# Kernel optimization log

Hardware: AMD Instinct MI355X
Metric: run time of the kernel (lower is better)

Reference implementation:

```python
import jax, jax.numpy as jnp
import numpy as np

B, T, H = 64, 1024, 1024


def setup_inputs() -> dict:
    key = jax.random.key(0)
    ks = jax.random.split(key, 8)
    s = 1.0 / np.sqrt(H)
    return {
        "spatial_feats": jax.random.normal(ks[0], (B, T, H), dtype=jnp.float32),
        "hidden_state": jax.random.normal(ks[1], (B, H), dtype=jnp.float32),
        "W_enc": jax.random.uniform(ks[2], (H, H), jnp.float32, -s, s),
        "b_enc": jax.random.uniform(ks[3], (H,), jnp.float32, -s, s),
        "W_dec": jax.random.uniform(ks[4], (H, H), jnp.float32, -s, s),
        "b_dec": jax.random.uniform(ks[5], (H,), jnp.float32, -s, s),
        "w_score": jax.random.uniform(ks[6], (H,), jnp.float32, -s, s),
        "b_score": jax.random.uniform(ks[7], (), jnp.float32, -s, s),
    }


def reference(spatial_feats, hidden_state, W_enc, b_enc, W_dec, b_dec, w_score, b_score):
    # decoder_proj(hidden_state): [B, H] -> [B, 1, H]
    dec = (jnp.einsum("bh,oh->bo", hidden_state, W_dec) + b_dec)[:, None, :]
    # encoder_proj(spatial_feats): [B, T, H]
    enc = jnp.einsum("bth,oh->bto", spatial_feats, W_enc) + b_enc
    energy = jnp.tanh(enc + dec)                      # [B, T, H]
    scores = jnp.einsum("bth,h->bt", energy, w_score) + b_score  # [B, T]
    weights = jax.nn.softmax(scores, axis=1)          # [B, T]
    context = jnp.einsum("bth,bt->bh", spatial_feats, weights)   # [B, H]
    return (context, weights)
```

## Files before the change

### kernel.cpp

```cpp
#include <hip/hip_runtime.h>
#include <hip/hip_bf16.h>
#include <math.h>


typedef __attribute__((ext_vector_type(8))) short bf16x8;
typedef __attribute__((ext_vector_type(8))) unsigned short ushort8;
typedef __attribute__((ext_vector_type(4))) float f32x4;

__device__ __forceinline__ unsigned short f2bf(float f) {
  union { float f; unsigned int u; } v; v.f = f;
  unsigned int r = v.u + 0x7FFFu + ((v.u >> 16) & 1u);
  return (unsigned short)(r >> 16);
}

__device__ __forceinline__ float bf2f(unsigned short b) {
  union { unsigned int u; float f; } v; v.u = ((unsigned int)b) << 16;
  return v.f;
}

__device__ __forceinline__ float fast_tanh(float x) {
  float e = __expf(2.0f * x);
  return 1.0f - 2.0f / (e + 1.0f);
}

__device__ __forceinline__ void gld16(const void* g, void* l) {
  __builtin_amdgcn_global_load_lds(
      (const __attribute__((address_space(1))) void*)g,
      (__attribute__((address_space(3))) void*)l, 16, 0, 0);
}

__global__ __launch_bounds__(256) void prep_kernel(
    const float* __restrict__ spatial, const float* __restrict__ hidden,
    const float* __restrict__ W_enc, const float* __restrict__ b_enc,
    const float* __restrict__ W_dec, const float* __restrict__ b_dec,
    unsigned short* __restrict__ Wbf, unsigned short* __restrict__ Abf,
    float* __restrict__ dec, int nCvt) {
  __shared__ float hs[1024];
  const int bid = blockIdx.x, tid = threadIdx.x;
  if (bid < nCvt) {
    const bool isW = bid < 32;
    const float* src = isW ? W_enc : spatial;
    unsigned short* dst = isW ? Wbf : Abf;
    const size_t base = (size_t)(isW ? bid : bid - 32) * 8192 + tid;
    #pragma unroll 4
    for (int i = 0; i < 32; i++) {
      size_t g4 = base + (size_t)i * 256;
      float4 v = ((const float4*)src)[g4];
      ushort4 o;
      o.x = f2bf(v.x); o.y = f2bf(v.y); o.z = f2bf(v.z); o.w = f2bf(v.w);
      *(ushort4*)(dst + g4 * 4) = o;
    }
    return;
  }
  const int dbid = bid - nCvt;
  const int b = dbid >> 3, o0 = (dbid & 7) * 128;
  const int wave = tid >> 6, lane = tid & 63;
  ((float4*)hs)[tid] = ((const float4*)(hidden + (size_t)b * 1024))[tid];
  __syncthreads();
  for (int it = 0; it < 32; it++) {
    int o = o0 + it * 4 + wave;
    const float4* w4 = (const float4*)(W_dec + (size_t)o * 1024);
    float4 acc; acc.x = acc.y = acc.z = acc.w = 0.f;
    #pragma unroll
    for (int j = 0; j < 4; j++) {
      int i = j * 64 + lane;
      float4 x = ((const float4*)hs)[i], y = w4[i];
      acc.x = fmaf(x.x, y.x, acc.x);
      acc.y = fmaf(x.y, y.y, acc.y);
      acc.z = fmaf(x.z, y.z, acc.z);
      acc.w = fmaf(x.w, y.w, acc.w);
    }
    float v = (acc.x + acc.y) + (acc.z + acc.w);
    #pragma unroll
    for (int off = 1; off < 64; off <<= 1) v += __shfl_xor(v, off);
    if (lane == 0) dec[b * 1024 + o] = v + b_dec[o] + b_enc[o];
  }
}

__global__ __launch_bounds__(256) void enc_score_bf16_kernel(
    const unsigned short* __restrict__ A,
    const unsigned short* __restrict__ W,
    const float* __restrict__ dec,
    const float* __restrict__ w_score,
    float* __restrict__ scores_p)
{
  __shared__ unsigned short As[3][128][32];
  __shared__ unsigned short Bs[3][128][32];

  const int bid = blockIdx.x;
  const int swz = (bid & 7) * 512 + (bid >> 3);
  const int n0 = (swz & 7) * 128;
  const int m0 = (swz >> 3) * 128;
  const int tid = threadIdx.x;
  const int lane = tid & 63, wave = tid >> 6;
  const int wm = (wave >> 1) * 64, wn = (wave & 1) * 64;
  const int quad = lane >> 4, colL = lane & 15;

  const int srow = wave * 32 + (lane >> 2);
  const int scol = (lane & 3) * 8;
  const unsigned short* ga = A + (size_t)(m0 + srow) * 1024 + scol;
  const unsigned short* gb = W + (size_t)(n0 + srow) * 1024 + scol;
  unsigned short* la = &As[0][0][0] + wave * 1024;
  unsigned short* lb = &Bs[0][0][0] + wave * 1024;

  f32x4 acc[4][4];
  #pragma unroll
  for (int mi = 0; mi < 4; mi++)
    #pragma unroll
    for (int ni = 0; ni < 4; ni++)
      acc[mi][ni] = (f32x4){0.f, 0.f, 0.f, 0.f};

  auto stage_tile = [&](int t, int b) {
    const unsigned short* ga_ = ga + t * 32;
    const unsigned short* gb_ = gb + t * 32;
    unsigned short* la_ = la + b * 4096;
    unsigned short* lb_ = lb + b * 4096;
    gld16(ga_,             la_);
    gld16(ga_ + 16 * 1024, la_ + 512);
    gld16(gb_,             lb_);
    gld16(gb_ + 16 * 1024, lb_ + 512);
  };

  auto compute_tile = [&](int b) {
    bf16x8 af[4], bfr[4];
    #pragma unroll
    for (int i = 0; i < 4; i++) {
      af[i]  = *(const bf16x8*)(&As[b][wm + i * 16 + colL][quad * 8]);
      bfr[i] = *(const bf16x8*)(&Bs[b][wn + i * 16 + colL][quad * 8]);
    }
    __builtin_amdgcn_s_setprio(1);
    #pragma unroll
    for (int mi = 0; mi < 4; mi++)
      #pragma unroll
      for (int ni = 0; ni < 4; ni++)
        acc[mi][ni] = __builtin_amdgcn_mfma_f32_16x16x32_bf16(
            af[mi], bfr[ni], acc[mi][ni], 0, 0, 0);
    __builtin_amdgcn_s_setprio(0);
  };

  stage_tile(0, 0);
  stage_tile(1, 1);

  int buf = 0;
  for (int t = 0; t < 31; t++) {
    asm volatile("s_waitcnt vmcnt(4)" ::: "memory");
    __builtin_amdgcn_s_barrier();
    if (t < 30) {
      int b2 = buf + 2; if (b2 >= 3) b2 -= 3;
      stage_tile(t + 2, b2);
    }
    compute_tile(buf);
    buf = (buf == 2) ? 0 : buf + 1;
  }
  asm volatile("s_waitcnt vmcnt(0)" ::: "memory");
  __builtin_amdgcn_s_barrier();
  compute_tile(buf);

  const int b = m0 >> 10;
  float decv[4], wsv[4];
  #pragma unroll
  for (int ni = 0; ni < 4; ni++) {
    int n = n0 + wn + ni * 16 + colL;
    decv[ni] = dec[b * 1024 + n];
    wsv[ni] = w_score[n];
  }
  const int slot = (swz & 7) * 2 + (wave & 1);
  #pragma unroll
  for (int mi = 0; mi < 4; mi++) {
    float rs[4] = {0.f, 0.f, 0.f, 0.f};
    #pragma unroll
    for (int ni = 0; ni < 4; ni++)
      #pragma unroll
      for (int r = 0; r < 4; r++)
        rs[r] += fast_tanh(acc[mi][ni][r] + decv[ni]) * wsv[ni];
    #pragma unroll
    for (int r = 0; r < 4; r++) {
      float v = rs[r];
      v += __shfl_xor(v, 1);
      v += __shfl_xor(v, 2);
      v += __shfl_xor(v, 4);
      v += __shfl_xor(v, 8);
      if (colL == 0)
        scores_p[slot * 65536 + m0 + wm + mi * 16 + quad * 4 + r] = v;
    }
  }
}

__global__ __launch_bounds__(256) void enc_score_f32_kernel(
    const float* __restrict__ A, const float* __restrict__ W,
    const float* __restrict__ dec, const float* __restrict__ w_score,
    float* __restrict__ scores_p) {
  __shared__ unsigned short As[128][32];
  __shared__ unsigned short Bs[128][32];
  const int bid = blockIdx.x;
  const int n0 = (bid & 7) * 128;
  const int m0 = (bid >> 3) * 128;
  const int tid = threadIdx.x;
  const int lane = tid & 63, wave = tid >> 6;
  const int wm = (wave >> 1) * 64, wn = (wave & 1) * 64;
  const int quad = lane >> 4, colL = lane & 15;
  const int srow = tid >> 3;
  const int scol = (tid & 7) * 4;
  f32x4 acc[4][4];
  #pragma unroll
  for (int mi = 0; mi < 4; mi++)
    #pragma unroll
    for (int ni = 0; ni < 4; ni++)
      acc[mi][ni] = (f32x4){0.f, 0.f, 0.f, 0.f};
  for (int k0 = 0; k0 < 1024; k0 += 32) {
    #pragma unroll
    for (int p = 0; p < 4; p++) {
      int r = p * 32 + srow;
      float4 va = *(const float4*)(A + (size_t)(m0 + r) * 1024 + (k0 + scol));
      float4 vb = *(const float4*)(W + (size_t)(n0 + r) * 1024 + (k0 + scol));
      ushort4 pa, pb;
      pa.x = f2bf(va.x); pa.y = f2bf(va.y); pa.z = f2bf(va.z); pa.w = f2bf(va.w);
      pb.x = f2bf(vb.x); pb.y = f2bf(vb.y); pb.z = f2bf(vb.z); pb.w = f2bf(vb.w);
      *(ushort4*)(&As[r][scol]) = pa;
      *(ushort4*)(&Bs[r][scol]) = pb;
    }
    __syncthreads();
    bf16x8 af[4], bfr[4];
    #pragma unroll
    for (int i = 0; i < 4; i++) {
      af[i]  = *(const bf16x8*)(&As[wm + i * 16 + colL][quad * 8]);
      bfr[i] = *(const bf16x8*)(&Bs[wn + i * 16 + colL][quad * 8]);
    }
    #pragma unroll
    for (int mi = 0; mi < 4; mi++)
      #pragma unroll
      for (int ni = 0; ni < 4; ni++)
        acc[mi][ni] = __builtin_amdgcn_mfma_f32_16x16x32_bf16(
            af[mi], bfr[ni], acc[mi][ni], 0, 0, 0);
    __syncthreads();
  }
  const int b = m0 >> 10;
  float decv[4], wsv[4];
  #pragma unroll
  for (int ni = 0; ni < 4; ni++) {
    int n = n0 + wn + ni * 16 + colL;
    decv[ni] = dec[b * 1024 + n];
    wsv[ni] = w_score[n];
  }
  const int slot = (bid & 7) * 2 + (wave & 1);
  #pragma unroll
  for (int mi = 0; mi < 4; mi++) {
    float rsv[4] = {0.f, 0.f, 0.f, 0.f};
    #pragma unroll
    for (int ni = 0; ni < 4; ni++)
      #pragma unroll
      for (int r = 0; r < 4; r++)
        rsv[r] += fast_tanh(acc[mi][ni][r] + decv[ni]) * wsv[ni];
    #pragma unroll
    for (int r = 0; r < 4; r++) {
      float v = rsv[r];
      v += __shfl_xor(v, 1);
      v += __shfl_xor(v, 2);
      v += __shfl_xor(v, 4);
      v += __shfl_xor(v, 8);
      if (colL == 0)
        scores_p[slot * 65536 + m0 + wm + mi * 16 + quad * 4 + r] = v;
    }
  }
}

__global__ void softmax_kernel(const float* __restrict__ scores_p,
                               float* __restrict__ weights,
                               float* __restrict__ context) {
  __shared__ float red[256];
  int b = blockIdx.x, tid = threadIdx.x;
  float4 z; z.x = z.y = z.z = z.w = 0.f;
  ((float4*)context)[blockIdx.x * 256 + tid] = z;
  float v[4];
  float mx = -1e30f;
  #pragma unroll
  for (int i = 0; i < 4; i++) {
    int m = b * 1024 + tid + i * 256;
    float s = 0.f;
    #pragma unroll
    for (int sl = 0; sl < 16; sl++) s += scores_p[sl * 65536 + m];
    v[i] = s;
    mx = fmaxf(mx, v[i]);
  }
  red[tid] = mx; __syncthreads();
  for (int off = 128; off > 0; off >>= 1) {
    if (tid < off) red[tid] = fmaxf(red[tid], red[tid + off]);
    __syncthreads();
  }
  mx = red[0]; __syncthreads();
  float sum = 0.f;
  #pragma unroll
  for (int i = 0; i < 4; i++) { v[i] = __expf(v[i] - mx); sum += v[i]; }
  red[tid] = sum; __syncthreads();
  for (int off = 128; off > 0; off >>= 1) {
    if (tid < off) red[tid] += red[tid + off];
    __syncthreads();
  }
  float inv = 1.0f / red[0];
  #pragma unroll
  for (int i = 0; i < 4; i++) weights[b * 1024 + tid + i * 256] = v[i] * inv;
}

__global__ void context_bf16_kernel(const unsigned short* __restrict__ Abf,
                                    const float* __restrict__ weights,
                                    float* __restrict__ context) {
  int b = blockIdx.x >> 3, tq = blockIdx.x & 7;
  int tid = threadIdx.x;
  __shared__ float wl[128];
  __shared__ float cs[128 * 8];
  if (tid < 128) wl[tid] = weights[b * 1024 + tq * 128 + tid];
  __syncthreads();
  const int hl = tid & 127, p = tid >> 7;
  const int h0 = hl * 8;
  const unsigned short* sp =
      Abf + ((size_t)(b * 1024 + tq * 128 + p)) * 1024 + h0;
  float acc[8];
  #pragma unroll
  for (int j = 0; j < 8; j++) acc[j] = 0.f;
  for (int t = 0; t < 128; t += 2) {
    float w = wl[t + p];
    ushort8 x = *(const ushort8*)(sp + (size_t)t * 1024);
    #pragma unroll
    for (int j = 0; j < 8; j++) acc[j] = fmaf(w, bf2f(x[j]), acc[j]);
  }
  if (p == 0) {
    #pragma unroll
    for (int j = 0; j < 8; j++) cs[hl * 8 + j] = acc[j];
  }
  __syncthreads();
  if (p == 1) {
    #pragma unroll
    for (int j = 0; j < 8; j++) cs[hl * 8 + j] += acc[j];
  }
  __syncthreads();
  if (p == 0) {
    #pragma unroll
    for (int j = 0; j < 8; j++)
      atomicAdd(&context[b * 1024 + h0 + j], cs[hl * 8 + j]);
  }
}

__global__ void context_f32_kernel(const float* __restrict__ spatial,
                                   const float* __restrict__ weights,
                                   float* __restrict__ context) {
  int b = blockIdx.x >> 3, tq = blockIdx.x & 7;
  int tid = threadIdx.x;
  __shared__ float wl[128];
  if (tid < 128) wl[tid] = weights[b * 1024 + tq * 128 + tid];
  __syncthreads();
  const float4* sp =
      (const float4*)(spatial + ((size_t)(b * 1024 + tq * 128)) * 1024);
  float4 acc; acc.x = acc.y = acc.z = acc.w = 0.f;
  #pragma unroll 4
  for (int t = 0; t < 128; t++) {
    float w = wl[t];
    float4 x = sp[(size_t)t * 256 + tid];
    acc.x = fmaf(w, x.x, acc.x);
    acc.y = fmaf(w, x.y, acc.y);
    acc.z = fmaf(w, x.z, acc.z);
    acc.w = fmaf(w, x.w, acc.w);
  }
  float* c = context + b * 1024 + tid * 4;
  atomicAdd(c + 0, acc.x);
  atomicAdd(c + 1, acc.y);
  atomicAdd(c + 2, acc.z);
  atomicAdd(c + 3, acc.w);
}

extern "C" void kernel_launch(void* const* d_in, const int* in_sizes, int n_in,
                              void* d_out, int out_size, void* d_ws, size_t ws_size,
                              hipStream_t stream) {
  const float* spatial  = (const float*)d_in[0];
  const float* hidden   = (const float*)d_in[1];
  const float* W_enc    = (const float*)d_in[2];
  const float* b_enc    = (const float*)d_in[3];
  const float* W_dec    = (const float*)d_in[4];
  const float* b_dec    = (const float*)d_in[5];
  const float* w_score  = (const float*)d_in[6];

  float* out      = (float*)d_out;
  float* context  = out;
  float* weights  = out + 65536;

  float* scores_p = (float*)d_ws;
  float* dec      = scores_p + 16 * 65536;
  unsigned short* Wbf = (unsigned short*)(dec + 65536);
  unsigned short* Abf = Wbf + 1024 * 1024;

  const size_t need =
      16ull * 65536 * 4 + 65536 * 4 + 2ull * 1024 * 1024 + 2ull * 65536 * 1024;

  if (ws_size >= need) {
    const int nCvt = 32 + 2048;
    prep_kernel<<<nCvt + 512, 256, 0, stream>>>(
        spatial, hidden, W_enc, b_enc, W_dec, b_dec, Wbf, Abf, dec, nCvt);
    enc_score_bf16_kernel<<<4096, 256, 0, stream>>>(Abf, Wbf, dec, w_score,
                                                    scores_p);
    softmax_kernel<<<64, 256, 0, stream>>>(scores_p, weights, context);
    context_bf16_kernel<<<512, 256, 0, stream>>>(Abf, weights, context);
  } else {
    prep_kernel<<<512, 256, 0, stream>>>(
        spatial, hidden, W_enc, b_enc, W_dec, b_dec, nullptr, nullptr, dec,
        0);
    enc_score_f32_kernel<<<4096, 256, 0, stream>>>(spatial, W_enc, dec,
                                                   w_score, scores_p);
    softmax_kernel<<<64, 256, 0, stream>>>(scores_p, weights, context);
    context_f32_kernel<<<512, 256, 0, stream>>>(spatial, weights, context);
  }
}
```

Before: 654.4 us.

## Enlarge encoder GEMM tiles to 256x256 with swizzled LDS and interleaved staging

Rewrites the fused encoder-projection/score GEMM to use 256x256 output tiles with K-step 64, eight waves per block, and double-buffered LDS laid out with an XOR swizzle. Global-to-LDS loads for the next K tiles are spread across the four compute sub-steps of each tile, so loads overlap the MFMA work. The larger tiles raise arithmetic intensity and cut the number of L2/HBM operand fetches. In exchange the kernel uses more LDS and registers (64 accumulators per thread), runs fewer blocks, and adds more barriers per K tile. The partial-score slot indexing is changed to match the new N tiling.

```diff
diff --git a/kernel.cpp b/kernel.cpp
--- a/kernel.cpp
+++ b/kernel.cpp
@@ -77,84 +77,109 @@
   }
 }
 
-__global__ __launch_bounds__(256) void enc_score_bf16_kernel(
+__global__ __launch_bounds__(512, 2) void enc_score_bf16_kernel(
     const unsigned short* __restrict__ A,
     const unsigned short* __restrict__ W,
     const float* __restrict__ dec,
     const float* __restrict__ w_score,
     float* __restrict__ scores_p)
 {
-  __shared__ unsigned short As[3][128][32];
-  __shared__ unsigned short Bs[3][128][32];
+  __shared__ unsigned short As[2][256][64];
+  __shared__ unsigned short Bs[2][256][64];
 
   const int bid = blockIdx.x;
-  const int swz = (bid & 7) * 512 + (bid >> 3);
-  const int n0 = (swz & 7) * 128;
-  const int m0 = (swz >> 3) * 128;
+  const int swz = (bid & 7) * 128 + (bid >> 3);
+  const int nt = swz & 3;
+  const int m0 = (swz >> 2) * 256;
+  const int n0 = nt * 256;
   const int tid = threadIdx.x;
   const int lane = tid & 63, wave = tid >> 6;
-  const int wm = (wave >> 1) * 64, wn = (wave & 1) * 64;
+  const int wm = (wave >> 2) * 128;
+  const int wn = (wave & 3) * 64;
   const int quad = lane >> 4, colL = lane & 15;
 
-  const int srow = wave * 32 + (lane >> 2);
-  const int scol = (lane & 3) * 8;
-  const unsigned short* ga = A + (size_t)(m0 + srow) * 1024 + scol;
-  const unsigned short* gb = W + (size_t)(n0 + srow) * 1024 + scol;
-  unsigned short* la = &As[0][0][0] + wave * 1024;
-  unsigned short* lb = &Bs[0][0][0] + wave * 1024;
-
-  f32x4 acc[4][4];
-  #pragma unroll
-  for (int mi = 0; mi < 4; mi++)
+  const int s_rowoff = wave * 16 + (lane >> 3);
+  const int s_col = ((lane & 7) ^ (lane >> 3)) * 8;
+  const unsigned short* gA = A + (size_t)m0 * 1024;
+  const unsigned short* gB = W + (size_t)n0 * 1024;
+
+  auto stageA = [&](int kt, int h) {
+    const unsigned short* src =
+        gA + (size_t)(h * 128 + s_rowoff) * 1024 + kt * 64 + s_col;
+    unsigned short* dst = &As[kt & 1][h * 128 + wave * 16][0];
+    gld16(src, dst);
+    gld16(src + 8 * 1024, dst + 8 * 64);
+  };
+  auto stageB = [&](int kt, int h) {
+    const unsigned short* src =
+        gB + (size_t)(h * 128 + s_rowoff) * 1024 + kt * 64 + s_col;
+    unsigned short* dst = &Bs[kt & 1][h * 128 + wave * 16][0];
+    gld16(src, dst);
+    gld16(src + 8 * 1024, dst + 8 * 64);
+  };
+
+  const int xs0 = ((0 * 4 + quad) ^ (colL & 7)) * 8;
+  const int xs1 = ((1 * 4 + quad) ^ (colL & 7)) * 8;
+
+  f32x4 acc[8][4];
+  #pragma unroll
+  for (int mi = 0; mi < 8; mi++)
     #pragma unroll
     for (int ni = 0; ni < 4; ni++)
       acc[mi][ni] = (f32x4){0.f, 0.f, 0.f, 0.f};
 
-  auto stage_tile = [&](int t, int b) {
-    const unsigned short* ga_ = ga + t * 32;
-    const unsigned short* gb_ = gb + t * 32;
-    unsigned short* la_ = la + b * 4096;
-    unsigned short* lb_ = lb + b * 4096;
-    gld16(ga_,             la_);
-    gld16(ga_ + 16 * 1024, la_ + 512);
-    gld16(gb_,             lb_);
-    gld16(gb_ + 16 * 1024, lb_ + 512);
+  stageA(0, 0); stageA(0, 1); stageB(0, 0); stageB(0, 1);
+  stageB(1, 0); stageB(1, 1);
+  asm volatile("s_waitcnt vmcnt(4)" ::: "memory");
+  __builtin_amdgcn_s_barrier();
+
+  auto ktile = [&](int kt, int buf) {
+    bf16x8 bfr[4][2];
+    #pragma unroll
+    for (int q = 0; q < 4; q++) {
+      bf16x8 af[2][2];
+      #pragma unroll
+      for (int mj = 0; mj < 2; mj++) {
+        const int row = wm + (q * 2 + mj) * 16 + colL;
+        af[mj][0] = *(const bf16x8*)&As[buf][row][xs0];
+        af[mj][1] = *(const bf16x8*)&As[buf][row][xs1];
+      }
+      if (q == 0) {
+        #pragma unroll
+        for (int ni = 0; ni < 4; ni++) {
+          const int row = wn + ni * 16 + colL;
+          bfr[ni][0] = *(const bf16x8*)&Bs[buf][row][xs0];
+          bfr[ni][1] = *(const bf16x8*)&Bs[buf][row][xs1];
+        }
+      }
+      if (q == 0 && kt + 1 < 16) stageA(kt + 1, 0);
+      if (q == 1 && kt + 1 < 16) stageA(kt + 1, 1);
+      if (q == 2 && kt + 2 < 16) stageB(kt + 2, 0);
+      if (q == 3 && kt + 2 < 16) stageB(kt + 2, 1);
+      __builtin_amdgcn_s_barrier();
+      asm volatile("s_waitcnt lgkmcnt(0)" ::: "memory");
+      __builtin_amdgcn_s_setprio(1);
+      #pragma unroll
+      for (int s = 0; s < 2; s++)
+        #pragma unroll
+        for (int mj = 0; mj < 2; mj++)
+          #pragma unroll
+          for (int ni = 0; ni < 4; ni++)
+            acc[q * 2 + mj][ni] = __builtin_amdgcn_mfma_f32_16x16x32_bf16(
+                af[mj][s], bfr[ni][s], acc[q * 2 + mj][ni], 0, 0, 0);
+      __builtin_amdgcn_s_setprio(0);
+      if (q == 3) {
+        if (kt + 2 < 16) asm volatile("s_waitcnt vmcnt(4)" ::: "memory");
+        else             asm volatile("s_waitcnt vmcnt(0)" ::: "memory");
+      }
+      __builtin_amdgcn_s_barrier();
+    }
   };
 
-  auto compute_tile = [&](int b) {
-    bf16x8 af[4], bfr[4];
-    #pragma unroll
-    for (int i = 0; i < 4; i++) {
-      af[i]  = *(const bf16x8*)(&As[b][wm + i * 16 + colL][quad * 8]);
-      bfr[i] = *(const bf16x8*)(&Bs[b][wn + i * 16 + colL][quad * 8]);
-    }
-    __builtin_amdgcn_s_setprio(1);
-    #pragma unroll
-    for (int mi = 0; mi < 4; mi++)
-      #pragma unroll
-      for (int ni = 0; ni < 4; ni++)
-        acc[mi][ni] = __builtin_amdgcn_mfma_f32_16x16x32_bf16(
-            af[mi], bfr[ni], acc[mi][ni], 0, 0, 0);
-    __builtin_amdgcn_s_setprio(0);
-  };
-
-  stage_tile(0, 0);
-  stage_tile(1, 1);
-
-  int buf = 0;
-  for (int t = 0; t < 31; t++) {
-    asm volatile("s_waitcnt vmcnt(4)" ::: "memory");
-    __builtin_amdgcn_s_barrier();
-    if (t < 30) {
-      int b2 = buf + 2; if (b2 >= 3) b2 -= 3;
-      stage_tile(t + 2, b2);
-    }
-    compute_tile(buf);
-    buf = (buf == 2) ? 0 : buf + 1;
-  }
-  asm volatile("s_waitcnt vmcnt(0)" ::: "memory");
-  __builtin_amdgcn_s_barrier();
-  compute_tile(buf);
+  for (int ku = 0; ku < 16; ku += 2) {
+    ktile(ku, 0);
+    ktile(ku + 1, 1);
+  }
 
   const int b = m0 >> 10;
   float decv[4], wsv[4];
@@ -164,9 +189,9 @@
     decv[ni] = dec[b * 1024 + n];
     wsv[ni] = w_score[n];
   }
-  const int slot = (swz & 7) * 2 + (wave & 1);
-  #pragma unroll
-  for (int mi = 0; mi < 4; mi++) {
+  const int slot = nt * 4 + (wave & 3);
+  #pragma unroll
+  for (int mi = 0; mi < 8; mi++) {
     float rs[4] = {0.f, 0.f, 0.f, 0.f};
     #pragma unroll
     for (int ni = 0; ni < 4; ni++)
@@ -394,7 +419,7 @@
     const int nCvt = 32 + 2048;
     prep_kernel<<<nCvt + 512, 256, 0, stream>>>(
         spatial, hidden, W_enc, b_enc, W_dec, b_dec, Wbf, Abf, dec, nCvt);
-    enc_score_bf16_kernel<<<4096, 256, 0, stream>>>(Abf, Wbf, dec, w_score,
+    enc_score_bf16_kernel<<<1024, 512, 0, stream>>>(Abf, Wbf, dec, w_score,
                                                     scores_p);
     softmax_kernel<<<64, 256, 0, stream>>>(scores_p, weights, context);
     context_bf16_kernel<<<512, 256, 0, stream>>>(Abf, weights, context);
```

After: 615.5 us. 5.9% less time.
